# Performance work log

Hardware: AMD Instinct MI355X
Metric: run time of the kernel (lower is better)

The kernel has to match this reference:

```python
import jax, jax.numpy as jnp
import numpy as np

N_ITEMS = 512
N_SAMPLES = 32768
WINDOW = 512
CHUNK = WINDOW // 2 + 1          # 257 rfft bins
N_COEFFS = CHUNK * 3             # 771: [mags | phases | start mags]
STEP = WINDOW // 2               # 256 hop
N_FRAMES = N_SAMPLES // STEP     # 128
BASE_RES = 0.5
SPAN = 1.0 - BASE_RES
EPS = 1e-12

_HANN = jnp.asarray(np.hanning(WINDOW), dtype=jnp.float32)


def setup_inputs() -> dict:
    key = jax.random.key(0)
    k1, k2, k3 = jax.random.split(key, 3)
    selections = jax.random.normal(k1, (8, 16, 4, N_ITEMS), dtype=jnp.float32)
    # init(x): uniform(-6, 6) * bernoulli(p=0.01)  -> sparse large-magnitude coeffs
    vals = jax.random.uniform(k2, (N_ITEMS, N_COEFFS), minval=-6.0, maxval=6.0, dtype=jnp.float32)
    mask = (jax.random.uniform(k3, (N_ITEMS, N_COEFFS)) < 0.01).astype(jnp.float32)
    items = vals * mask
    return {"selections": selections, "items": items}


def _resonance_synth(coeffs):
    # coeffs: (B, E, X, N_COEFFS)
    mags = BASE_RES + jax.nn.sigmoid(coeffs[..., :CHUNK]) * 0.9999 * SPAN       # decay per frame, in (0.5, 1)
    phases = jnp.tanh(coeffs[..., CHUNK:2 * CHUNK]) * jnp.pi                    # per-frame phase advance
    starts = jax.nn.sigmoid(coeffs[..., 2 * CHUNK:])                            # initial bin magnitudes

    # log-space cumulative decay scan across frames: mag at frame t = mags ** (t+1)
    t = jnp.arange(1, N_FRAMES + 1, dtype=jnp.float32)                          # (F,)
    log_m = jnp.log(mags + EPS)                                                 # (B,E,X,C)
    decay = jnp.exp(log_m[..., None, :] * t[:, None])                           # (B,E,X,F,C)
    phi = phases[..., None, :] * t[:, None]                                     # cumulative phase rotation

    spec = (starts[..., None, :] * decay).astype(jnp.complex64) * jnp.exp(1j * phi.astype(jnp.complex64))
    frames = jnp.fft.irfft(spec, n=WINDOW, axis=-1).astype(jnp.float32)         # (B,E,X,F,W)
    frames = frames * _HANN

    first = frames[..., :STEP]                                                  # (B,E,X,F,STEP)
    second = frames[..., STEP:]
    shifted = jnp.concatenate([jnp.zeros_like(second[..., :1, :]), second[..., :-1, :]], axis=-2)
    out = first + shifted                                                       # (B,E,X,F,STEP)
    return out.reshape(*frames.shape[:-2], N_FRAMES * STEP)                     # (B,E,X,N_SAMPLES)


def reference(selections, items):
    # select_items with selection_type='relu': non-negative mixture over the item table
    selected = jnp.einsum('bexi,ic->bexc', jax.nn.relu(selections), items)      # (B,E,X,N_COEFFS)
    res = _resonance_synth(selected)                                            # (B,E,X,N_SAMPLES)
    norm = jnp.linalg.norm(res, axis=-1, keepdims=True)
    return res / (norm + 1e-8)                                                  # unit_norm along samples
```

## Files before the change

kernel.cpp:

```cpp
#include <hip/hip_runtime.h>
#include <math.h>

#define N_ROWS   512
#define NBINS    257
#define N_COEFFS 771
#define STEP     256
#define N_FRAMES 128
#define N_SAMP   32768
#define KDIM     576
#define NCHUNK   18
#define PCH      9
#define PCOLS    288
#define TWO_PI   6.283185307179586f
#define PADN     32
#define CSC_BLKS 13

typedef _Float16 half8 __attribute__((ext_vector_type(8)));
typedef float floatx4 __attribute__((ext_vector_type(4)));

__global__ __launch_bounds__(256) void k_pre(const float* __restrict__ items,
                                             int* __restrict__ idx,
                                             float* __restrict__ val,
                                             _Float16* __restrict__ Bt) {
    const int bid = blockIdx.x;
    const int tid = threadIdx.x;
    if (bid >= CSC_BLKS) {
        int jg = bid - CSC_BLKS;
        int n  = ((jg >> 7) << 6) + (jg & 63) + (((jg >> 6) & 1) << 8);
        for (int k = tid; k < KDIM; k += 256) {
            float v = 0.f;
            if (k < NBINS) {
                int r = (k * n) & 511;
                v = cosf(TWO_PI * (float)r * (1.f / 512.f));
            } else if (k < 2 * NBINS) {
                int r = ((k - NBINS) * n) & 511;
                v = -sinf(TWO_PI * (float)r * (1.f / 512.f));
            }
            size_t pos = ((size_t)((k >> 5) * 4 + ((k >> 3) & 3)) * 512 + jg) * 8 + (k & 7);
            Bt[pos] = (_Float16)v;
        }
        return;
    }
    __shared__ float tile[64][65];
    __shared__ int   basec[64];
    const int c0   = bid * 64;
    const int w    = tid >> 6;
    const int lane = tid & 63;
    const int c    = c0 + lane;
    if (tid < 64) basec[tid] = 0;
    for (int r0 = 0; r0 < 512; r0 += 64) {
        float v[16];
        #pragma unroll
        for (int rr = 0; rr < 16; ++rr)
            v[rr] = (c < N_COEFFS) ? items[(size_t)(r0 + rr * 4 + w) * N_COEFFS + c] : 0.f;
        #pragma unroll
        for (int rr = 0; rr < 16; ++rr)
            tile[rr * 4 + w][lane] = v[rr];
        __syncthreads();
        #pragma unroll
        for (int cc = 0; cc < 16; ++cc) {
            int cl   = w * 16 + cc;
            int gcol = c0 + cl;
            float x  = tile[lane][cl];
            unsigned long long m = __ballot(x != 0.f);
            int base = basec[cl];
            int pos  = base + __popcll(m & ((1ull << lane) - 1ull));
            if (gcol < N_COEFFS && x != 0.f && pos < PADN) {
                idx[gcol * PADN + pos] = r0 + lane;
                val[gcol * PADN + pos] = x;
            }
            if (lane == 0) basec[cl] = base + __popcll(m);
        }
        __syncthreads();
    }
    for (int j = tid; j < 64 * PADN; j += 256) {
        int cl = j >> 5, pz = j & (PADN - 1);
        int gcol = c0 + cl;
        if (gcol < N_COEFFS) {
            int b = basec[cl]; b = b < PADN ? b : PADN;
            if (pz >= b) {
                idx[gcol * PADN + pz] = 0;
                val[gcol * PADN + pz] = 0.f;
            }
        }
    }
}

__global__ __launch_bounds__(256) void k_params(const float* __restrict__ sel,
                                                const int* __restrict__ csc_idx,
                                                const float* __restrict__ csc_val,
                                                float4* __restrict__ pa,
                                                float2* __restrict__ pb) {
    int row = blockIdx.x;
    int tid = threadIdx.x;
    __shared__ float s[512];
    float v0 = sel[row * 512 + tid];
    float v1 = sel[row * 512 + tid + 256];
    s[tid]       = v0 > 0.f ? v0 : 0.f;
    s[tid + 256] = v1 > 0.f ? v1 : 0.f;
    __syncthreads();
    for (int k = tid; k < NBINS; k += 256) {
        float acc[3];
        #pragma unroll
        for (int ch = 0; ch < 3; ++ch) {
            int cc = ch * NBINS + k;
            const int*   ip = csc_idx + cc * PADN;
            const float* vp = csc_val + cc * PADN;
            float a = 0.f;
            #pragma unroll
            for (int j = 0; j < PADN; ++j)
                a = fmaf(s[ip[j]], vp[j], a);
            acc[ch] = a;
        }
        float cm = acc[0], cp = acc[1], cs = acc[2];
        float sig_m = 1.f / (1.f + expf(-cm));
        float mag   = 0.5f + sig_m * 0.9999f * 0.5f;
        float lm    = logf(mag + 1e-12f);
        float ph    = tanhf(cp) * 3.14159265358979323846f;
        float sph, cph;
        sincosf(ph, &sph, &cph);
        float st = 1.f / (1.f + expf(-cs));
        float w  = (k == 0 || k == 256) ? (1.f / 512.f) : (2.f / 512.f);
        int indx = row * NBINS + k;
        pa[indx] = make_float4(lm, ph, cph, sph);
        pb[indx] = make_float2(st * w, mag);
    }
}

__global__ __launch_bounds__(512, 2) void k_row(const float4* __restrict__ pa,
                                                const float2* __restrict__ pb,
                                                const _Float16* __restrict__ basis,
                                                float* __restrict__ out) {
    __shared__ _Float16 Asm[PCH * 4096];
    __shared__ _Float16 Bsm[2][16384];
    __shared__ float    SBB[4][64];
    __shared__ float    red[8];

    const int row  = blockIdx.x;
    const int t    = threadIdx.x;
    const int lane = t & 63;
    const int w    = t >> 6;
    const int wm   = w >> 2;
    const int wn   = w & 3;
    const int quad = lane >> 4;
    const int l16  = lane & 15;

    auto agen = [&](int ph) {
        if (t < PCOLS) {
            int gc = ph * PCOLS + t;
            int bin; bool isCos;
            if (gc < NBINS)          { bin = gc;          isCos = true;  }
            else if (gc < 2 * NBINS) { bin = gc - NBINS;  isCos = false; }
            else                     { bin = 0;           isCos = true;  }
            float4 P = pa[row * NBINS + bin];
            float2 Q = pb[row * NBINS + bin];
            float D = 512.f * Q.x * Q.y;
            if (gc >= 2 * NBINS) D = 0.f;
            float c = P.z, s = P.w;
            int ch = t >> 5, g = (t >> 3) & 3, o = t & 7;
            _Float16* base = &Asm[ch * 4096 + o];
            for (int f = 0; f < N_FRAMES; ++f) {
                float val = isCos ? D * c : D * s;
                base[f * 32 + ((g ^ ((f >> 1) & 3) ^ ((f >> 3) & 3)) << 3)] = (_Float16)val;
                D *= Q.y;
                float nc = fmaf(c, P.z, -s * P.w);
                float ns = fmaf(s, P.z,  c * P.w);
                c = nc; s = ns;
            }
        }
    };

    half8 L[4];
    #pragma unroll
    for (int g = 0; g < 4; ++g)
        L[g] = *(const half8*)(basis + ((size_t)(0 * 4 + g) * 512 + t) * 8);
    agen(0);
    #pragma unroll
    for (int g = 0; g < 4; ++g)
        *(half8*)&Bsm[0][g * 4096 + t * 8] = L[g];
    #pragma unroll
    for (int g = 0; g < 4; ++g)
        L[g] = *(const half8*)(basis + ((size_t)(1 * 4 + g) * 512 + t) * 8);
    __syncthreads();

    floatx4 acc[4][8] = {};
    int p = 0;
    for (int ph = 0; ph < 2; ++ph) {
        if (ph == 1) { agen(1); __syncthreads(); }
        for (int ks = 0; ks < PCH; ++ks) {
            int gc = ph * PCH + ks;
            if (gc < NCHUNK - 1) {
                #pragma unroll
                for (int g = 0; g < 4; ++g)
                    *(half8*)&Bsm[p ^ 1][g * 4096 + t * 8] = L[g];
                if (gc < NCHUNK - 2) {
                    #pragma unroll
                    for (int g = 0; g < 4; ++g)
                        L[g] = *(const half8*)(basis + ((size_t)((gc + 2) * 4 + g) * 512 + t) * 8);
                }
            }
            half8 av[4];
            #pragma unroll
            for (int mt = 0; mt < 4; ++mt) {
                int m = wm * 64 + mt * 16 + l16;
                av[mt] = *(const half8*)&Asm[ks * 4096 + m * 32 +
                          ((quad ^ ((m >> 1) & 3) ^ ((m >> 3) & 3)) << 3)];
            }
            #pragma unroll
            for (int nt = 0; nt < 8; ++nt) {
                int u = wn * 128 + nt * 16 + l16;
                half8 bv = *(const half8*)&Bsm[p][quad * 4096 + u * 8];
                #pragma unroll
                for (int mt = 0; mt < 4; ++mt)
                    acc[mt][nt] = __builtin_amdgcn_mfma_f32_16x16x32_f16(av[mt], bv, acc[mt][nt], 0, 0, 0);
            }
            __syncthreads();
            p ^= 1;
        }
    }

    float h1[4], h2[4];
    #pragma unroll
    for (int nt = 0; nt < 4; ++nt) {
        int n1 = wn * 64 + nt * 16 + l16;
        h1[nt] = 0.5f - 0.5f * cosf(TWO_PI * (float)n1 / 511.f);
        h2[nt] = 0.5f - 0.5f * cosf(TWO_PI * (float)(n1 + 256) / 511.f);
    }
    if (wm == 0 && quad == 3) {
        #pragma unroll
        for (int nt = 0; nt < 4; ++nt)
            SBB[wn][nt * 16 + l16] = acc[3][nt + 4][3] * h2[nt];
    }
    __syncthreads();

    float oreg[4][4][4];
    float prevLast[4] = {0.f, 0.f, 0.f, 0.f};
    float ssq = 0.f;
    #pragma unroll
    for (int mt = 0; mt < 4; ++mt) {
        #pragma unroll
        for (int nt = 0; nt < 4; ++nt) {
            float W2[4];
            #pragma unroll
            for (int rr = 0; rr < 4; ++rr) W2[rr] = acc[mt][nt + 4][rr] * h2[nt];
            float tmp = (quad == 3) ? prevLast[nt] : W2[3];
            float carry = __shfl(tmp, (lane + 48) & 63, 64);
            if (mt == 0 && quad == 0)
                carry = (wm == 1) ? SBB[wn][nt * 16 + l16] : 0.f;
            float v = fmaf(acc[mt][nt][0], h1[nt], carry);
            oreg[mt][nt][0] = v; ssq = fmaf(v, v, ssq);
            #pragma unroll
            for (int rr = 1; rr < 4; ++rr) {
                v = fmaf(acc[mt][nt][rr], h1[nt], W2[rr - 1]);
                oreg[mt][nt][rr] = v; ssq = fmaf(v, v, ssq);
            }
            prevLast[nt] = W2[3];
        }
    }

    #pragma unroll
    for (int off = 32; off > 0; off >>= 1) ssq += __shfl_down(ssq, off, 64);
    if (lane == 0) red[w] = ssq;
    __syncthreads();
    float tot = red[0] + red[1] + red[2] + red[3] + red[4] + red[5] + red[6] + red[7];
    float scale = 1.f / (sqrtf(tot) + 1e-8f);

    float* orow = out + (size_t)row * N_SAMP;
    #pragma unroll
    for (int mt = 0; mt < 4; ++mt) {
        #pragma unroll
        for (int nt = 0; nt < 4; ++nt) {
            int n1 = wn * 64 + nt * 16 + l16;
            #pragma unroll
            for (int rr = 0; rr < 4; ++rr) {
                int f = wm * 64 + mt * 16 + quad * 4 + rr;
                orow[f * 256 + n1] = oreg[mt][nt][rr] * scale;
            }
        }
    }
}

extern "C" void kernel_launch(void* const* d_in, const int* in_sizes, int n_in,
                              void* d_out, int out_size, void* d_ws, size_t ws_size,
                              hipStream_t stream) {
    const float* sel   = (const float*)d_in[0];
    const float* items = (const float*)d_in[1];
    float* out = (float*)d_out;

    char* ws = (char*)d_ws;
    size_t off = 0;
    float4* pa   = (float4*)(ws + off); off += (size_t)N_ROWS * NBINS * 16;   off = (off + 255) & ~255ull;
    float2* pb   = (float2*)(ws + off); off += (size_t)N_ROWS * NBINS * 8;    off = (off + 255) & ~255ull;
    _Float16* basis = (_Float16*)(ws + off); off += (size_t)NCHUNK * 4 * 512 * 8 * 2; off = (off + 255) & ~255ull;
    int*   csc_idx = (int*)(ws + off);   off += (size_t)N_COEFFS * PADN * 4;  off = (off + 255) & ~255ull;
    float* csc_val = (float*)(ws + off); off += (size_t)N_COEFFS * PADN * 4;

    k_pre<<<dim3(CSC_BLKS + 512), dim3(256), 0, stream>>>(items, csc_idx, csc_val, basis);
    k_params<<<dim3(N_ROWS), dim3(256), 0, stream>>>(sel, csc_idx, csc_val, pa, pb);
    k_row<<<dim3(N_ROWS), dim3(512), 0, stream>>>(pa, pb, basis, out);
}
```

Baseline: 171.8 us.

## Fold Hann window and overlap-add into basis, fuse params into row kernel

Pre-multiplies the Hann window into the inverse-DFT basis and builds the overlap-add as a second GEMM term against the previous frame's spectrum (shifted A rows), so each output sample comes straight out of the MFMA accumulator. The params kernel is fused into the row kernel, removing the pa/pb workspace round trip and one launch. B fragments are now read directly from global/L2 instead of being double-buffered through LDS, which shrinks LDS and allows three blocks per CU. The cost is double the MFMA count per output and reliance on cache for B loads.

```diff
diff --git a/kernel.cpp b/kernel.cpp
--- a/kernel.cpp
+++ b/kernel.cpp
@@ -3,17 +3,17 @@
 
 #define N_ROWS   512
 #define NBINS    257
-#define N_COEFFS 771
-#define STEP     256
+#define KPAD     576
+#define NCHUNKB  36
+#define PCH      9
+#define PCOLS    288
+#define NOUT     256
 #define N_FRAMES 128
 #define N_SAMP   32768
-#define KDIM     576
-#define NCHUNK   18
-#define PCH      9
-#define PCOLS    288
 #define TWO_PI   6.283185307179586f
 #define PADN     32
 #define CSC_BLKS 13
+#define N_COEFFS 771
 
 typedef _Float16 half8 __attribute__((ext_vector_type(8)));
 typedef float floatx4 __attribute__((ext_vector_type(4)));
@@ -25,18 +25,21 @@
     const int bid = blockIdx.x;
     const int tid = threadIdx.x;
     if (bid >= CSC_BLKS) {
-        int jg = bid - CSC_BLKS;
-        int n  = ((jg >> 7) << 6) + (jg & 63) + (((jg >> 6) & 1) << 8);
-        for (int k = tid; k < KDIM; k += 256) {
-            float v = 0.f;
+        int n1 = bid - CSC_BLKS;
+        for (int kk = tid; kk < 2 * KPAD; kk += 256) {
+            int half = kk >= KPAD;
+            int k    = kk - half * KPAD;
+            int s    = n1 + half * 256;
+            float w  = 0.5f - 0.5f * cosf(TWO_PI * (float)s / 511.f);
+            float v  = 0.f;
             if (k < NBINS) {
-                int r = (k * n) & 511;
-                v = cosf(TWO_PI * (float)r * (1.f / 512.f));
+                int r = (k * s) & 511;
+                v = cosf(TWO_PI * (float)r * (1.f / 512.f)) * w;
             } else if (k < 2 * NBINS) {
-                int r = ((k - NBINS) * n) & 511;
-                v = -sinf(TWO_PI * (float)r * (1.f / 512.f));
-            }
-            size_t pos = ((size_t)((k >> 5) * 4 + ((k >> 3) & 3)) * 512 + jg) * 8 + (k & 7);
+                int r = ((k - NBINS) * s) & 511;
+                v = -sinf(TWO_PI * (float)r * (1.f / 512.f)) * w;
+            }
+            size_t pos = ((size_t)((kk >> 5) * 4 + ((kk >> 3) & 3)) * NOUT + n1) * 8 + (kk & 7);
             Bt[pos] = (_Float16)v;
         }
         return;
@@ -86,54 +89,13 @@
     }
 }
 
-__global__ __launch_bounds__(256) void k_params(const float* __restrict__ sel,
+__global__ __launch_bounds__(512, 3) void k_row(const float* __restrict__ sel,
                                                 const int* __restrict__ csc_idx,
                                                 const float* __restrict__ csc_val,
-                                                float4* __restrict__ pa,
-                                                float2* __restrict__ pb) {
-    int row = blockIdx.x;
-    int tid = threadIdx.x;
-    __shared__ float s[512];
-    float v0 = sel[row * 512 + tid];
-    float v1 = sel[row * 512 + tid + 256];
-    s[tid]       = v0 > 0.f ? v0 : 0.f;
-    s[tid + 256] = v1 > 0.f ? v1 : 0.f;
-    __syncthreads();
-    for (int k = tid; k < NBINS; k += 256) {
-        float acc[3];
-        #pragma unroll
-        for (int ch = 0; ch < 3; ++ch) {
-            int cc = ch * NBINS + k;
-            const int*   ip = csc_idx + cc * PADN;
-            const float* vp = csc_val + cc * PADN;
-            float a = 0.f;
-            #pragma unroll
-            for (int j = 0; j < PADN; ++j)
-                a = fmaf(s[ip[j]], vp[j], a);
-            acc[ch] = a;
-        }
-        float cm = acc[0], cp = acc[1], cs = acc[2];
-        float sig_m = 1.f / (1.f + expf(-cm));
-        float mag   = 0.5f + sig_m * 0.9999f * 0.5f;
-        float lm    = logf(mag + 1e-12f);
-        float ph    = tanhf(cp) * 3.14159265358979323846f;
-        float sph, cph;
-        sincosf(ph, &sph, &cph);
-        float st = 1.f / (1.f + expf(-cs));
-        float w  = (k == 0 || k == 256) ? (1.f / 512.f) : (2.f / 512.f);
-        int indx = row * NBINS + k;
-        pa[indx] = make_float4(lm, ph, cph, sph);
-        pb[indx] = make_float2(st * w, mag);
-    }
-}
-
-__global__ __launch_bounds__(512, 2) void k_row(const float4* __restrict__ pa,
-                                                const float2* __restrict__ pb,
                                                 const _Float16* __restrict__ basis,
                                                 float* __restrict__ out) {
     __shared__ _Float16 Asm[PCH * 4096];
-    __shared__ _Float16 Bsm[2][16384];
-    __shared__ float    SBB[4][64];
+    __shared__ float    par[NBINS * 4];
     __shared__ float    red[8];
 
     const int row  = blockIdx.x;
@@ -145,6 +107,40 @@
     const int quad = lane >> 4;
     const int l16  = lane & 15;
 
+    {
+        float* s = (float*)Asm;
+        float v0 = sel[row * 512 + t];
+        s[t] = v0 > 0.f ? v0 : 0.f;
+        __syncthreads();
+        if (t < NBINS) {
+            float acc3[3];
+            #pragma unroll
+            for (int ch = 0; ch < 3; ++ch) {
+                int cc = ch * NBINS + t;
+                const int*   ip = csc_idx + cc * PADN;
+                const float* vp = csc_val + cc * PADN;
+                float a = 0.f;
+                #pragma unroll
+                for (int j = 0; j < PADN; ++j)
+                    a = fmaf(s[ip[j]], vp[j], a);
+                acc3[ch] = a;
+            }
+            float sig_m = 1.f / (1.f + expf(-acc3[0]));
+            float mag   = 0.5f + sig_m * 0.9999f * 0.5f;
+            float ph    = tanhf(acc3[1]) * 3.14159265358979323846f;
+            float sph, cph;
+            sincosf(ph, &sph, &cph);
+            float st  = 1.f / (1.f + expf(-acc3[2]));
+            float wgt = (t == 0 || t == 256) ? (1.f / 512.f) : (2.f / 512.f);
+            float qx  = st * wgt;
+            par[t * 4 + 0] = cph;
+            par[t * 4 + 1] = sph;
+            par[t * 4 + 2] = mag;
+            par[t * 4 + 3] = 512.f * qx * mag;
+        }
+        __syncthreads();
+    }
+
     auto agen = [&](int ph) {
         if (t < PCOLS) {
             int gc = ph * PCOLS + t;
@@ -152,112 +148,70 @@
             if (gc < NBINS)          { bin = gc;          isCos = true;  }
             else if (gc < 2 * NBINS) { bin = gc - NBINS;  isCos = false; }
             else                     { bin = 0;           isCos = true;  }
-            float4 P = pa[row * NBINS + bin];
-            float2 Q = pb[row * NBINS + bin];
-            float D = 512.f * Q.x * Q.y;
+            float cph = par[bin * 4 + 0];
+            float sph = par[bin * 4 + 1];
+            float mag = par[bin * 4 + 2];
+            float D   = par[bin * 4 + 3];
             if (gc >= 2 * NBINS) D = 0.f;
-            float c = P.z, s = P.w;
+            float c = cph, s = sph;
             int ch = t >> 5, g = (t >> 3) & 3, o = t & 7;
             _Float16* base = &Asm[ch * 4096 + o];
             for (int f = 0; f < N_FRAMES; ++f) {
                 float val = isCos ? D * c : D * s;
                 base[f * 32 + ((g ^ ((f >> 1) & 3) ^ ((f >> 3) & 3)) << 3)] = (_Float16)val;
-                D *= Q.y;
-                float nc = fmaf(c, P.z, -s * P.w);
-                float ns = fmaf(s, P.z,  c * P.w);
+                D *= mag;
+                float nc = fmaf(c, cph, -s * sph);
+                float ns = fmaf(s, cph,  c * sph);
                 c = nc; s = ns;
             }
         }
     };
 
-    half8 L[4];
-    #pragma unroll
-    for (int g = 0; g < 4; ++g)
-        L[g] = *(const half8*)(basis + ((size_t)(0 * 4 + g) * 512 + t) * 8);
-    agen(0);
-    #pragma unroll
-    for (int g = 0; g < 4; ++g)
-        *(half8*)&Bsm[0][g * 4096 + t * 8] = L[g];
-    #pragma unroll
-    for (int g = 0; g < 4; ++g)
-        L[g] = *(const half8*)(basis + ((size_t)(1 * 4 + g) * 512 + t) * 8);
-    __syncthreads();
-
-    floatx4 acc[4][8] = {};
-    int p = 0;
+    const _Float16* bbase = basis + ((size_t)quad * NOUT + wn * 64 + l16) * 8;
+
+    floatx4 acc[4][4] = {};
+    const half8 hz = {};
+
     for (int ph = 0; ph < 2; ++ph) {
-        if (ph == 1) { agen(1); __syncthreads(); }
+        if (ph == 0) { agen(0); }
+        else         { __syncthreads(); agen(1); }
+        __syncthreads();
         for (int ks = 0; ks < PCH; ++ks) {
-            int gc = ph * PCH + ks;
-            if (gc < NCHUNK - 1) {
-                #pragma unroll
-                for (int g = 0; g < 4; ++g)
-                    *(half8*)&Bsm[p ^ 1][g * 4096 + t * 8] = L[g];
-                if (gc < NCHUNK - 2) {
-                    #pragma unroll
-                    for (int g = 0; g < 4; ++g)
-                        L[g] = *(const half8*)(basis + ((size_t)((gc + 2) * 4 + g) * 512 + t) * 8);
-                }
-            }
-            half8 av[4];
+            const int cb0 = ph * PCH + ks;
+            const int cb1 = cb0 + 18;
+            half8 av[4], avs[4];
             #pragma unroll
             for (int mt = 0; mt < 4; ++mt) {
-                int m = wm * 64 + mt * 16 + l16;
+                int m  = wm * 64 + mt * 16 + l16;
                 av[mt] = *(const half8*)&Asm[ks * 4096 + m * 32 +
                           ((quad ^ ((m >> 1) & 3) ^ ((m >> 3) & 3)) << 3)];
-            }
-            #pragma unroll
-            for (int nt = 0; nt < 8; ++nt) {
-                int u = wn * 128 + nt * 16 + l16;
-                half8 bv = *(const half8*)&Bsm[p][quad * 4096 + u * 8];
+                int ms = m - 1; if (ms < 0) ms = 0;
+                avs[mt] = *(const half8*)&Asm[ks * 4096 + ms * 32 +
+                          ((quad ^ ((ms >> 1) & 3) ^ ((ms >> 3) & 3)) << 3)];
+            }
+            if (wm == 0 && l16 == 0) avs[0] = hz;
+            #pragma unroll
+            for (int nt = 0; nt < 4; ++nt) {
+                half8 bv  = *(const half8*)(bbase + (size_t)cb0 * 8192 + nt * 128);
+                half8 bvs = *(const half8*)(bbase + (size_t)cb1 * 8192 + nt * 128);
                 #pragma unroll
                 for (int mt = 0; mt < 4; ++mt)
-                    acc[mt][nt] = __builtin_amdgcn_mfma_f32_16x16x32_f16(av[mt], bv, acc[mt][nt], 0, 0, 0);
-            }
-            __syncthreads();
-            p ^= 1;
-        }
-    }
-
-    float h1[4], h2[4];
-    #pragma unroll
-    for (int nt = 0; nt < 4; ++nt) {
-        int n1 = wn * 64 + nt * 16 + l16;
-        h1[nt] = 0.5f - 0.5f * cosf(TWO_PI * (float)n1 / 511.f);
-        h2[nt] = 0.5f - 0.5f * cosf(TWO_PI * (float)(n1 + 256) / 511.f);
-    }
-    if (wm == 0 && quad == 3) {
-        #pragma unroll
-        for (int nt = 0; nt < 4; ++nt)
-            SBB[wn][nt * 16 + l16] = acc[3][nt + 4][3] * h2[nt];
-    }
-    __syncthreads();
-
-    float oreg[4][4][4];
-    float prevLast[4] = {0.f, 0.f, 0.f, 0.f};
+                    acc[mt][nt] = __builtin_amdgcn_mfma_f32_16x16x32_f16(av[mt],  bv,  acc[mt][nt], 0, 0, 0);
+                #pragma unroll
+                for (int mt = 0; mt < 4; ++mt)
+                    acc[mt][nt] = __builtin_amdgcn_mfma_f32_16x16x32_f16(avs[mt], bvs, acc[mt][nt], 0, 0, 0);
+            }
+        }
+    }
+
     float ssq = 0.f;
     #pragma unroll
-    for (int mt = 0; mt < 4; ++mt) {
-        #pragma unroll
-        for (int nt = 0; nt < 4; ++nt) {
-            float W2[4];
-            #pragma unroll
-            for (int rr = 0; rr < 4; ++rr) W2[rr] = acc[mt][nt + 4][rr] * h2[nt];
-            float tmp = (quad == 3) ? prevLast[nt] : W2[3];
-            float carry = __shfl(tmp, (lane + 48) & 63, 64);
-            if (mt == 0 && quad == 0)
-                carry = (wm == 1) ? SBB[wn][nt * 16 + l16] : 0.f;
-            float v = fmaf(acc[mt][nt][0], h1[nt], carry);
-            oreg[mt][nt][0] = v; ssq = fmaf(v, v, ssq);
-            #pragma unroll
-            for (int rr = 1; rr < 4; ++rr) {
-                v = fmaf(acc[mt][nt][rr], h1[nt], W2[rr - 1]);
-                oreg[mt][nt][rr] = v; ssq = fmaf(v, v, ssq);
-            }
-            prevLast[nt] = W2[3];
-        }
-    }
-
+    for (int mt = 0; mt < 4; ++mt)
+        #pragma unroll
+        for (int nt = 0; nt < 4; ++nt)
+            #pragma unroll
+            for (int rr = 0; rr < 4; ++rr)
+                ssq = fmaf(acc[mt][nt][rr], acc[mt][nt][rr], ssq);
     #pragma unroll
     for (int off = 32; off > 0; off >>= 1) ssq += __shfl_down(ssq, off, 64);
     if (lane == 0) red[w] = ssq;
@@ -274,7 +228,7 @@
             #pragma unroll
             for (int rr = 0; rr < 4; ++rr) {
                 int f = wm * 64 + mt * 16 + quad * 4 + rr;
-                orow[f * 256 + n1] = oreg[mt][nt][rr] * scale;
+                orow[f * 256 + n1] = acc[mt][nt][rr] * scale;
             }
         }
     }
@@ -289,13 +243,10 @@
 
     char* ws = (char*)d_ws;
     size_t off = 0;
-    float4* pa   = (float4*)(ws + off); off += (size_t)N_ROWS * NBINS * 16;   off = (off + 255) & ~255ull;
-    float2* pb   = (float2*)(ws + off); off += (size_t)N_ROWS * NBINS * 8;    off = (off + 255) & ~255ull;
-    _Float16* basis = (_Float16*)(ws + off); off += (size_t)NCHUNK * 4 * 512 * 8 * 2; off = (off + 255) & ~255ull;
+    _Float16* basis = (_Float16*)(ws + off); off += (size_t)NCHUNKB * 4 * NOUT * 8 * 2; off = (off + 255) & ~255ull;
     int*   csc_idx = (int*)(ws + off);   off += (size_t)N_COEFFS * PADN * 4;  off = (off + 255) & ~255ull;
     float* csc_val = (float*)(ws + off); off += (size_t)N_COEFFS * PADN * 4;
 
-    k_pre<<<dim3(CSC_BLKS + 512), dim3(256), 0, stream>>>(items, csc_idx, csc_val, basis);
-    k_params<<<dim3(N_ROWS), dim3(256), 0, stream>>>(sel, csc_idx, csc_val, pa, pb);
-    k_row<<<dim3(N_ROWS), dim3(512), 0, stream>>>(pa, pb, basis, out);
+    k_pre<<<dim3(CSC_BLKS + NOUT), dim3(256), 0, stream>>>(items, csc_idx, csc_val, basis);
+    k_row<<<dim3(N_ROWS), dim3(512), 0, stream>>>(sel, csc_idx, csc_val, basis, out);
 }
```

After: 206.8 us. +20.4%, slower.
